# Kernel tuning notes

Measured on AMD Instinct MI355X. Metric: run time of the kernel, lower is better.

The kernel has to match this reference:

```python
import jax, jax.numpy as jnp
import numpy as np
from jax import lax

_R2 = 1.0 / np.sqrt(2.0)
_L = np.array([_R2, _R2]); _Hf = np.array([-_R2, _R2])
F_LL = jnp.asarray(np.outer(_L, _L), jnp.float32)
F_LH = jnp.asarray(np.outer(_L, _Hf), jnp.float32)
F_HL = jnp.asarray(np.outer(_Hf, _L), jnp.float32)
F_HH = jnp.asarray(np.outer(_Hf, _Hf), jnp.float32)
EPS = 1e-5


def _up2(x, f):
    # grouped ConvTranspose2d(k=2, s=2): out[n,c,2i+a,2j+b] = x[n,c,i,j] * f[a,b]
    n, c, h, w = x.shape
    return (x[:, :, :, None, :, None] * f[None, None, None, :, None, :]).reshape(n, c, 2 * h, 2 * w)


def _wave_unpool(ll, lh, hl, hh):
    return _up2(ll, F_LL) + _up2(lh, F_LH) + _up2(hl, F_HL) + _up2(hh, F_HH)


def _rpad(x):
    return jnp.pad(x, ((0, 0), (0, 0), (1, 1), (1, 1)), mode='reflect')


def _conv_relu(x, w, b):
    y = lax.conv_general_dilated(_rpad(x), w, (1, 1), 'VALID',
                                 dimension_numbers=('NCHW', 'OIHW', 'NCHW'))
    return jax.nn.relu(y + b[None, :, None, None])


def _masked_stats(feat, mask):
    # per-(class,n,c) mean/std over NONZERO elements of feat*mask (mask binary)
    nz = (feat != 0).astype(feat.dtype)           # [N,C,H,W]
    cnt = jnp.einsum('khw,nchw->knc', mask, nz)
    s1 = jnp.einsum('khw,nchw->knc', mask, feat)
    s2 = jnp.einsum('khw,nchw->knc', mask, feat * feat)
    m = s1 / jnp.maximum(cnt, 1.0)
    v = (s2 - cnt * m * m) / jnp.maximum(cnt - 1.0, 1.0) + EPS  # unbiased var + eps
    return m, jnp.sqrt(v)


def _global_stats(feat):
    nz = (feat != 0).astype(feat.dtype)
    cnt = nz.sum((2, 3))
    s1 = feat.sum((2, 3))
    s2 = (feat * feat).sum((2, 3))
    m = s1 / jnp.maximum(cnt, 1.0)
    v = (s2 - cnt * m * m) / jnp.maximum(cnt - 1.0, 1.0) + EPS
    return m, jnp.sqrt(v)


def _adain_per_class(content, style, cmask, smask):
    # c_ds=True, s_ds=True branch of AdaIN_per_class, vectorized over classes.
    hc, wc = content.shape[2], content.shape[3]
    hs, ws = style.shape[2], style.shape[3]
    cm = cmask[:, ::2, ::2][:, :hc, :wc]   # MaxPool2d(k=1,s=2) == strided slice
    sm = smask[:, ::2, ::2][:, :hs, :ws]
    cfe = content + EPS
    sfe = style + EPS
    flags = (cmask.max((1, 2)) != 0).astype(content.dtype)   # skip empty content classes
    s_empty = (smask.max((1, 2)) == 0)                       # style-mask-empty -> global style stats
    smm, ssm = _masked_stats(sfe, sm)       # [K,N,C]
    smu, ssu = _global_stats(sfe)           # [N,C]
    s_mean = jnp.where(s_empty[:, None, None], smu[None], smm)
    s_std = jnp.where(s_empty[:, None, None], ssu[None], ssm)
    c_mean, c_std = _masked_stats(cfe, cm)
    # res = sum_k cm_k * ((cfe*cm_k - c_mean)/c_std * s_std + s_mean)
    #     = cfe * sum_k cm_k*scale_k + sum_k cm_k*shift_k   (cm binary)
    scale = flags[:, None, None] * s_std / c_std
    shift = flags[:, None, None] * (s_mean - c_mean * s_std / c_std)
    return cfe * jnp.einsum('khw,knc->nchw', cm, scale) + jnp.einsum('khw,knc->nchw', cm, shift)


def setup_inputs() -> dict:
    key = jax.random.key(0)
    ks = iter(jax.random.split(key, 64))

    def rn(shape, scale=1.0):
        return jax.random.normal(next(ks), shape, jnp.float32) * scale

    inp = {}
    inp['f1'] = rn((4, 128, 128, 128))
    inp['f2'] = rn((4, 512, 32, 32))
    for nm, sh in [('s2', (4, 256, 32, 32)), ('s1', (4, 128, 64, 64)), ('s0', (4, 64, 128, 128))]:
        for band in ('lh', 'hl', 'hh'):
            inp[nm + '_' + band] = rn(sh)
    inp['content_mask'] = jax.random.randint(next(ks), (8, 256, 256), 0, 2).astype(jnp.float32)
    inp['style_mask'] = jax.random.randint(next(ks), (8, 256, 256), 0, 2).astype(jnp.float32)
    for nm, (o, i) in [('w11', (512, 512)), ('w12', (256, 512)), ('w21', (256, 256)),
                       ('w22', (256, 256)), ('w23', (256, 256)), ('w24', (128, 256)),
                       ('w31', (128, 128)), ('w32', (128, 128)), ('w33', (64, 128))]:
        inp[nm] = rn((o, i, 3, 3), 1.0 / np.sqrt(9.0 * i))
        inp['b' + nm[1:]] = jnp.zeros((o,), jnp.float32)
    return inp


def reference(f1, f2, s2_lh, s2_hl, s2_hh, s1_lh, s1_hl, s1_hh, s0_lh, s0_hl, s0_hh,
              content_mask, style_mask,
              w11, b11, w12, b12, w21, b21, w22, b22, w23, b23, w24, b24,
              w31, b31, w32, b32, w33, b33):
    out = _conv_relu(f2, w11, b11)
    out = _conv_relu(out, w12, b12)
    out = _wave_unpool(out, s2_lh, s2_hl, s2_hh)
    out = _rpad(out)[:, :, :s1_hh.shape[2], :s1_hh.shape[3]]
    out = _conv_relu(out, w21, b21)
    out = _conv_relu(out, w22, b22)
    out = _conv_relu(out, w23, b23)
    out = _conv_relu(out, w24, b24)
    out = _wave_unpool(out, s1_lh, s1_hl, s1_hh)
    out = _rpad(out)[:, :, :f1.shape[2], :f1.shape[3]]
    out = _adain_per_class(out, f1, content_mask, style_mask)
    out = _conv_relu(out, w31, b31)
    out = _conv_relu(out, w32, b32)
    out = _conv_relu(out, w33, b33)
    out = _wave_unpool(out, s0_lh, s0_hl, s0_hh)
    return _rpad(out)
```

## Files before the change

### kernel.cpp

```cpp
#include <hip/hip_runtime.h>

#define EPSF 1e-5f

typedef __attribute__((ext_vector_type(4)))  short short4v;
typedef __attribute__((ext_vector_type(8)))  short short8;
typedef __attribute__((ext_vector_type(4)))  float f32x4;
typedef __attribute__((ext_vector_type(16))) float f32x16;

__device__ __forceinline__ unsigned short f2bf(float f) {
  unsigned u = __builtin_bit_cast(unsigned, f);
  unsigned r = (u + 0x7FFFu + ((u >> 16) & 1u)) >> 16;
  return (unsigned short)r;
}
__device__ __forceinline__ float bf2f(unsigned short h) {
  unsigned u = ((unsigned)h) << 16;
  return __builtin_bit_cast(float, u);
}

__global__ void wt_prep(const float* __restrict__ w, unsigned short* __restrict__ wt,
                        int C, int K) {
  int C8 = C >> 3;
  int idx = blockIdx.x * 256 + threadIdx.x;
  if (idx >= K * C8) return;
  int k = idx / C8, ch = idx - k * C8;
  int tap = blockIdx.y;
  const float* src = w + ((size_t)k * C + ch * 8) * 9 + tap;
  short8 v;
#pragma unroll
  for (int cl = 0; cl < 8; ++cl) v[cl] = (short)f2bf(src[cl * 9]);
  *(short8*)(wt + ((size_t)(tap * C8 + ch) * K + k) * 8) = v;
}

__global__ void nchw_to_nc8(const float* __restrict__ in, unsigned short* __restrict__ out,
                            int C8, int HW, int total) {
  int idx = blockIdx.x * 256 + threadIdx.x;
  if (idx >= total) return;
  int pix = idx % HW; int t = idx / HW; int ch = t % C8; int n = t / C8;
  const float* s = in + ((size_t)(n * C8 + ch) * 8) * HW + pix;
  short8 v;
#pragma unroll
  for (int cl = 0; cl < 8; ++cl) v[cl] = (short)f2bf(s[(size_t)cl * HW]);
  *(short8*)(out + (size_t)idx * 8) = v;
}

__global__ __launch_bounds__(256) void conv3x3_mfma(
    const unsigned short* __restrict__ act, const unsigned short* __restrict__ wt,
    const float* __restrict__ bias, unsigned short* __restrict__ out,
    unsigned short* __restrict__ partial, int C, int K, int H, int W, int S) {
  const int C8 = C >> 3, K8 = K >> 3;
  const int HW = H * W;
  const int tid = threadIdx.x;
  const int lane = tid & 63, wid = tid >> 6;
  const int l31 = lane & 31, lhi = lane >> 5;
  const int w0 = blockIdx.x * 16, h0 = blockIdx.y * 16;
  const int kbn = K >> 6;
  int zz = blockIdx.z;
  const int sp = zz % S; zz /= S;
  const int kb = zz % kbn;
  const int n  = zz / kbn;
  const int k0 = kb * 64;

  __shared__ __align__(16) unsigned short smem[24576];
  __shared__ float sbias[64];
  if (tid < 64) sbias[tid] = bias[k0 + tid];

  int g16[6];
#pragma unroll
  for (int it = 0; it < 6; ++it) {
    int slot = it * 256 + wid * 64 + lane;
    int s = slot < 1296 ? slot : 0;
    int chi = s / 324; int r = s - chi * 324;
    int y = r / 18, x = r - y * 18;
    int gy = h0 - 1 + y; gy = gy < 0 ? -gy : (gy >= H ? 2 * H - 2 - gy : gy);
    int gx = w0 - 1 + x; gx = gx < 0 ? -gx : (gx >= W ? 2 * W - 2 - gx : gx);
    g16[it] = ((n * C8 + chi) * H + gy) * W + gx;
  }

  const int pbase = wid * 64;
  int pb[2];
#pragma unroll
  for (int nf = 0; nf < 2; ++nf) {
    int p = pbase + nf * 32 + l31;
    pb[nf] = (p >> 4) * 18 + (p & 15);
  }
  int bb8[2][2];
#pragma unroll
  for (int ks = 0; ks < 2; ++ks)
#pragma unroll
    for (int nf = 0; nf < 2; ++nf)
      bb8[ks][nf] = ((ks * 2 + lhi) * 324 + pb[nf]) * 8;

  const size_t tapStep   = (size_t)C8 * K * 8;
  const size_t chunkStep = (size_t)4 * K * 8;
  const int cps = (C >> 5) / S;
  const int c0 = sp * cps;
  const unsigned short* ap[2][2];
#pragma unroll
  for (int ks = 0; ks < 2; ++ks)
#pragma unroll
    for (int mf = 0; mf < 2; ++mf)
      ap[ks][mf] = wt + ((size_t)(c0 * 4) * K
                  + (size_t)((ks * 2 + lhi) * K + k0 + mf * 32 + l31)) * 8;

  f32x16 acc[2][2] = {};

#define STAGE(BSEL, CI)                                                          \
  {                                                                              \
    _Pragma("unroll")                                                            \
    for (int it = 0; it < 6; ++it) {                                             \
      const unsigned short* g = act + ((size_t)g16[it] + (size_t)(CI) * 4 * HW) * 8; \
      __builtin_amdgcn_global_load_lds(                                          \
          (const __attribute__((address_space(1))) unsigned int*)g,              \
          (__attribute__((address_space(3))) unsigned int*)                      \
              &smem[(BSEL) * 12288 + (it * 256 + wid * 64) * 8],                 \
          16, 0, 0);                                                             \
    }                                                                            \
  }

  STAGE(0, c0)

  for (int i = 0; i < cps; ++i) {
    __syncthreads();
    const int boff = (i & 1) * 12288;
    const unsigned short* aw[2][2];
    short8 acur[2][2], anx[2][2];
#pragma unroll
    for (int ks = 0; ks < 2; ++ks)
#pragma unroll
      for (int mf = 0; mf < 2; ++mf) {
        aw[ks][mf] = ap[ks][mf];
        acur[ks][mf] = *(const short8*)aw[ks][mf];
        aw[ks][mf] += tapStep;
      }
#pragma unroll
    for (int tap = 0; tap < 9; ++tap) {
      if (tap < 8) {
#pragma unroll
        for (int ks = 0; ks < 2; ++ks)
#pragma unroll
          for (int mf = 0; mf < 2; ++mf) {
            anx[ks][mf] = *(const short8*)aw[ks][mf];
            aw[ks][mf] += tapStep;
          }
      }
      if (tap == 7 && i + 1 < cps) STAGE((i & 1) ^ 1, c0 + i + 1)
      const int ty = tap / 3, txx = tap - ty * 3;
      const int toff = (ty * 18 + txx) * 8;
      short8 b[2][2];
#pragma unroll
      for (int ks = 0; ks < 2; ++ks)
#pragma unroll
        for (int nf = 0; nf < 2; ++nf)
          b[nf][ks] = *(const short8*)&smem[boff + bb8[ks][nf] + toff];
#pragma unroll
      for (int ks = 0; ks < 2; ++ks)
#pragma unroll
        for (int mf = 0; mf < 2; ++mf)
#pragma unroll
          for (int nf = 0; nf < 2; ++nf)
            acc[mf][nf] = __builtin_amdgcn_mfma_f32_32x32x16_bf16(
                acur[ks][mf], b[nf][ks], acc[mf][nf], 0, 0, 0);
#pragma unroll
      for (int ks = 0; ks < 2; ++ks)
#pragma unroll
        for (int mf = 0; mf < 2; ++mf)
          acur[ks][mf] = anx[ks][mf];
    }
#pragma unroll
    for (int ks = 0; ks < 2; ++ks)
#pragma unroll
      for (int mf = 0; mf < 2; ++mf)
        ap[ks][mf] += chunkStep;
  }

  if (S > 1) {
    unsigned short* P = partial + (size_t)sp * ((size_t)4 * K * HW);
#pragma unroll
    for (int mf = 0; mf < 2; ++mf)
#pragma unroll
      for (int nf = 0; nf < 2; ++nf) {
        int p = pbase + nf * 32 + l31;
        int gp = (h0 + (p >> 4)) * W + (w0 + (p & 15));
#pragma unroll
        for (int q = 0; q < 4; ++q) {
          size_t ad = ((size_t)(n * K8 + (k0 >> 3) + mf * 4 + q) * HW + gp) * 8 + 4 * lhi;
          short4v v = { (short)f2bf(acc[mf][nf][4 * q]),
                        (short)f2bf(acc[mf][nf][4 * q + 1]),
                        (short)f2bf(acc[mf][nf][4 * q + 2]),
                        (short)f2bf(acc[mf][nf][4 * q + 3]) };
          *(short4v*)(P + ad) = v;
        }
      }
    return;
  }

  __syncthreads();
#pragma unroll
  for (int mf = 0; mf < 2; ++mf)
#pragma unroll
    for (int nf = 0; nf < 2; ++nf) {
      int pix = pbase + nf * 32 + l31;
#pragma unroll
      for (int rp = 0; rp < 8; ++rp) {
        const int r0 = rp * 2;
        int row0 = (r0 & 3) + 8 * (r0 >> 2) + 4 * lhi;
        int c64 = mf * 32 + row0;
        float v0 = acc[mf][nf][r0]     + sbias[c64];
        float v1 = acc[mf][nf][r0 + 1] + sbias[c64 + 1];
        v0 = v0 > 0.f ? v0 : 0.f;
        v1 = v1 > 0.f ? v1 : 0.f;
        unsigned pk = (unsigned)f2bf(v0) | ((unsigned)f2bf(v1) << 16);
        int chh = mf * 4 + (r0 >> 2);
        int clo = (r0 & 3) + 4 * lhi;
        *(unsigned*)&smem[((chh * 256 + pix) * 8 + clo)] = pk;
      }
    }
  __syncthreads();
#pragma unroll
  for (int i = 0; i < 8; ++i) {
    int slot = i * 256 + tid;
    int ch = slot >> 8;
    int p = slot & 255;
    int py = p >> 4, px = p & 15;
    short8 v = *(const short8*)&smem[slot * 8];
    *(short8*)(out + (((size_t)(n * K8 + (k0 >> 3) + ch) * H + h0 + py) * W + w0 + px) * 8) = v;
  }
#undef STAGE
}

__global__ void combine_bias_relu(const unsigned short* __restrict__ P,
                                  const float* __restrict__ bias,
                                  unsigned short* __restrict__ out, int S, int K8, int HW,
                                  int total8) {
  int idx = blockIdx.x * 256 + threadIdx.x;
  if (idx >= total8) return;
  int k8 = (idx / HW) % K8;
  const unsigned short* p = P + (size_t)idx * 8;
  size_t stride = (size_t)total8 * 8;
  float v[8];
#pragma unroll
  for (int c = 0; c < 8; ++c) v[c] = bf2f(p[c]);
  for (int s = 1; s < S; ++s) {
#pragma unroll
    for (int c = 0; c < 8; ++c) v[c] += bf2f(p[(size_t)s * stride + c]);
  }
  short8 r;
#pragma unroll
  for (int c = 0; c < 8; ++c) {
    float x = v[c] + bias[k8 * 8 + c];
    x = x > 0.f ? x : 0.f;
    r[c] = (short)f2bf(x);
  }
  *(short8*)(out + (size_t)idx * 8) = r;
}

__global__ void unpool_shift_fused(const unsigned short* __restrict__ P,
                                   const float* __restrict__ bias,
                                   const float* __restrict__ lh, const float* __restrict__ hl,
                                   const float* __restrict__ hh, unsigned short* __restrict__ out,
                                   int C8, int Hh, int Wh, int S, int total) {
  int idx = blockIdx.x * 256 + threadIdx.x;
  if (idx >= total) return;
  const int Ho = 2 * Hh, Wo = 2 * Wh;
  int j = idx % Wo; int t = idx / Wo;
  int i = t % Ho; t /= Ho;
  int ch = t % C8; int n = t / C8;
  int si = (i == 0) ? 1 : i - 1;
  int sj = (j == 0) ? 1 : j - 1;
  float sa = (si & 1) ? 1.f : -1.f;
  float sb = (sj & 1) ? 1.f : -1.f;
  int hy = si >> 1, hx = sj >> 1;
  size_t HWh = (size_t)Hh * Wh;
  const size_t sstr = (size_t)4 * (C8 * 8) * HWh;
  size_t lbase = ((size_t)(n * C8 + ch) * HWh + hy * Wh + hx) * 8;
  float ll[8];
  {
    short8 v0 = *(const short8*)(P + lbase);
#pragma unroll
    for (int cl = 0; cl < 8; ++cl) ll[cl] = bf2f((unsigned short)v0[cl]);
  }
  for (int s = 1; s < S; ++s) {
    short8 vs = *(const short8*)(P + (size_t)s * sstr + lbase);
#pragma unroll
    for (int cl = 0; cl < 8; ++cl) ll[cl] += bf2f((unsigned short)vs[cl]);
  }
#pragma unroll
  for (int cl = 0; cl < 8; ++cl) {
    float x = ll[cl] + bias[ch * 8 + cl];
    ll[cl] = x > 0.f ? x : 0.f;
  }
  size_t bb = ((size_t)(n * C8 + ch) * 8 * Hh + hy) * Wh + hx;
  short8 res;
#pragma unroll
  for (int cl = 0; cl < 8; ++cl) {
    float v = 0.5f * (ll[cl] + sb * lh[bb + cl * HWh] + sa * hl[bb + cl * HWh]
                      + sa * sb * hh[bb + cl * HWh]);
    res[cl] = (short)f2bf(v);
  }
  *(short8*)(out + (size_t)idx * 8) = res;
}

__global__ void unpool_rpad_final_v3(const unsigned short* __restrict__ ll,
                                     const float* __restrict__ lh, const float* __restrict__ hl,
                                     const float* __restrict__ hh, float* __restrict__ out) {
  const int img = blockIdx.y;
  int idx = blockIdx.x * 256 + threadIdx.x;
  if (idx >= 130 * 129) return;
  int g = idx / 129, jm = idx - g * 129;
  const int n = img >> 6, c = img & 63;

  int hy = (g == 0) ? 0 : (g == 129 ? 127 : g - 1);
  int hx0 = (jm == 0) ? 0 : jm - 1;
  int hx1 = (jm == 128) ? 127 : jm;

  size_t lb = ((size_t)(n * 8 + (c >> 3)) * 16384 + hy * 128) * 8 + (c & 7);
  float ll0 = bf2f(ll[lb + hx0 * 8]);
  float ll1 = bf2f(ll[lb + hx1 * 8]);

  size_t bb = ((size_t)img * 128 + hy) * 128;
  float l0 = lh[bb + hx0], G0 = hl[bb + hx0], h0 = hh[bb + hx0];
  float l1 = lh[bb + hx1], G1 = hl[bb + hx1], h1 = hh[bb + hx1];

  float e0 = ll0 + l0, f0 = G0 + h0;
  float e1 = ll1 - l1, f1 = G1 - h1;
  float2 rm = make_float2(0.5f * (e0 - f0), 0.5f * (e1 - f1));
  float2 rp = make_float2(0.5f * (e0 + f0), 0.5f * (e1 + f1));

  float* obase = out + (size_t)img * 258 * 258 + 2 * jm;
  if (g == 0) {
    *(float2*)&obase[0] = rp;
  } else if (g == 129) {
    *(float2*)&obase[(size_t)257 * 258] = rm;
  } else {
    *(float2*)&obase[(size_t)(2 * g - 1) * 258] = rm;
    *(float2*)&obase[(size_t)(2 * g) * 258]     = rp;
  }
}

__global__ void pack_masks(const float* __restrict__ cmask, const float* __restrict__ smask,
                           unsigned* __restrict__ cbits, unsigned* __restrict__ sbits) {
  int idx = blockIdx.x * 256 + threadIdx.x;
  if (idx >= 16384) return;
  int h = idx >> 7, w = idx & 127;
  unsigned cb = 0, sb = 0;
#pragma unroll
  for (int k = 0; k < 8; ++k) {
    int off = (k * 256 + 2 * h) * 256 + 2 * w;
    if (cmask[off] != 0.f) cb |= (1u << k);
    if (smask[off] != 0.f) sb |= (1u << k);
  }
  cbits[idx] = cb;
  sbits[idx] = sb;
}

__global__ __launch_bounds__(1024) void mask_flags(
    const float* __restrict__ cmask, const float* __restrict__ smask,
    float* __restrict__ flagc, float* __restrict__ sany) {
  int k = blockIdx.x;
  const float* cm = cmask + (size_t)k * 65536;
  const float* sm = smask + (size_t)k * 65536;
  int ca = 0, sa = 0;
  for (int i = threadIdx.x; i < 65536; i += 1024) {
    ca |= (cm[i] != 0.f);
    sa |= (sm[i] != 0.f);
  }
#pragma unroll
  for (int off = 32; off > 0; off >>= 1) {
    ca |= __shfl_xor(ca, off, 64);
    sa |= __shfl_xor(sa, off, 64);
  }
  __shared__ int rc[16], rs[16];
  int wv = threadIdx.x >> 6;
  if ((threadIdx.x & 63) == 0) { rc[wv] = ca; rs[wv] = sa; }
  __syncthreads();
  if (threadIdx.x == 0) {
    int c = 0, s = 0;
#pragma unroll
    for (int i = 0; i < 16; ++i) { c |= rc[i]; s |= rs[i]; }
    flagc[k] = c ? 1.f : 0.f;
    sany[k]  = s ? 1.f : 0.f;
  }
}

__global__ __launch_bounds__(256) void masked_stats_bf16(
    const unsigned short* __restrict__ feat, const unsigned* __restrict__ bits,
    float* __restrict__ outp, int NC) {
  constexpr int NV = 24;
  int b = blockIdx.x; int n = b >> 7, c = b & 127;
  const int sp = blockIdx.y;
  const unsigned short* f = feat + (size_t)(n * 16 + (c >> 3)) * 16384 * 8 + (c & 7);
  float acc[NV];
#pragma unroll
  for (int j = 0; j < NV; ++j) acc[j] = 0.f;
  const int p0 = sp * 4096;
  for (int it = 0; it < 16; ++it) {
    int i = p0 + it * 256 + threadIdx.x;
    float v = bf2f(f[(size_t)i * 8]) + EPSF;
    float nz = (v != 0.f) ? 1.f : 0.f;
    float v2 = v * v;
    unsigned m = bits[i];
#pragma unroll
    for (int k = 0; k < 8; ++k) {
      float mk = (float)((m >> k) & 1u);
      acc[k * 3 + 0] += mk * nz;
      acc[k * 3 + 1] += mk * v;
      acc[k * 3 + 2] += mk * v2;
    }
  }
#pragma unroll
  for (int j = 0; j < NV; ++j) {
    float v = acc[j];
#pragma unroll
    for (int off = 32; off > 0; off >>= 1) v += __shfl_xor(v, off, 64);
    acc[j] = v;
  }
  __shared__ float red[4][NV];
  int lane = threadIdx.x & 63, wv = threadIdx.x >> 6;
  if (lane == 0) {
#pragma unroll
    for (int j = 0; j < NV; ++j) red[wv][j] = acc[j];
  }
  __syncthreads();
  int tid = threadIdx.x;
  if (tid < NV) {
    float s = red[0][tid] + red[1][tid] + red[2][tid] + red[3][tid];
    outp[(sp * NV + tid) * NC + b] = s;
  }
}

__global__ __launch_bounds__(256) void masked_stats_f32g(
    const float* __restrict__ feat, const unsigned* __restrict__ bits,
    float* __restrict__ sstp, float* __restrict__ gstp, int NC) {
  constexpr int NV = 27;
  const int b = blockIdx.x;
  const int sp = blockIdx.y;
  const float* f = feat + (size_t)b * 16384;
  float acc[NV];
#pragma unroll
  for (int j = 0; j < NV; ++j) acc[j] = 0.f;
  const int p0 = sp * 4096;
#pragma unroll 1
  for (int it = 0; it < 4; ++it) {
    int p = p0 + it * 1024 + threadIdx.x * 4;
    float4 v4 = *(const float4*)&f[p];
    uint4 m4 = *(const uint4*)&bits[p];
#pragma unroll
    for (int e = 0; e < 4; ++e) {
      float v = (&v4.x)[e] + EPSF;
      unsigned m = (&m4.x)[e];
      float nz = (v != 0.f) ? 1.f : 0.f;
      float v2 = v * v;
#pragma unroll
      for (int k = 0; k < 8; ++k) {
        float mk = (float)((m >> k) & 1u);
        acc[k * 3 + 0] += mk * nz;
        acc[k * 3 + 1] += mk * v;
        acc[k * 3 + 2] += mk * v2;
      }
      acc[24] += nz; acc[25] += v; acc[26] += v2;
    }
  }
#pragma unroll
  for (int j = 0; j < NV; ++j) {
    float v = acc[j];
#pragma unroll
    for (int off = 32; off > 0; off >>= 1) v += __shfl_xor(v, off, 64);
    acc[j] = v;
  }
  __shared__ float red[4][NV];
  int lane = threadIdx.x & 63, wv = threadIdx.x >> 6;
  if (lane == 0) {
#pragma unroll
    for (int j = 0; j < NV; ++j) red[wv][j] = acc[j];
  }
  __syncthreads();
  int tid = threadIdx.x;
  if (tid < NV) {
    float s = red[0][tid] + red[1][tid] + red[2][tid] + red[3][tid];
    if (tid < 24) sstp[(sp * 24 + tid) * NC + b] = s;
    else gstp[(sp * 3 + (tid - 24)) * NC + b] = s;
  }
}

__global__ void finalize_ss(const float* __restrict__ cstp, const float* __restrict__ sstp,
                            const float* __restrict__ gstp, const float* __restrict__ flagc,
                            const float* __restrict__ sany,
                            float* __restrict__ scal, float* __restrict__ shft, int NC) {
  int idx = blockIdx.x * blockDim.x + threadIdx.x;
  if (idx >= 8 * NC) return;
  int k = idx / NC, b = idx - k * NC;
  bool useg = (sany[k] == 0.f);
  float ccnt = 0.f, cs1 = 0.f, cs2 = 0.f, scnt = 0.f, ss1 = 0.f, ss2 = 0.f;
#pragma unroll
  for (int s = 0; s < 4; ++s) {
    const float* cp = cstp + s * 24 * NC;
    ccnt += cp[(k * 3 + 0) * NC + b];
    cs1  += cp[(k * 3 + 1) * NC + b];
    cs2  += cp[(k * 3 + 2) * NC + b];
    if (useg) {
      const float* gp = gstp + s * 3 * NC;
      scnt += gp[0 * NC + b]; ss1 += gp[1 * NC + b]; ss2 += gp[2 * NC + b];
    } else {
      const float* spp = sstp + s * 24 * NC;
      scnt += spp[(k * 3 + 0) * NC + b];
      ss1  += spp[(k * 3 + 1) * NC + b];
      ss2  += spp[(k * 3 + 2) * NC + b];
    }
  }
  float cmn  = cs1 / fmaxf(ccnt, 1.f);
  float cvv  = (cs2 - ccnt * cmn * cmn) / fmaxf(ccnt - 1.f, 1.f) + EPSF;
  float cstd = sqrtf(cvv);
  float smn  = ss1 / fmaxf(scnt, 1.f);
  float svv  = (ss2 - scnt * smn * smn) / fmaxf(scnt - 1.f, 1.f) + EPSF;
  float sstd = sqrtf(svv);
  float fl = flagc[k];
  float r  = sstd / cstd;
  scal[idx] = fl * r;
  shft[idx] = fl * (smn - cmn * r);
}

__global__ void adain_apply_nc8(const unsigned short* __restrict__ content,
                                const unsigned* __restrict__ bits,
                                const float* __restrict__ scal, const float* __restrict__ shft,
                                unsigned short* __restrict__ out) {
  int ch = blockIdx.x & 15, n = blockIdx.x >> 4;
  __shared__ float ssc[8][8], ssh[8][8];
  if (threadIdx.x < 64) {
    int k = threadIdx.x >> 3, cl = threadIdx.x & 7;
    int c = ch * 8 + cl;
    ssc[k][cl] = scal[k * 512 + n * 128 + c];
    ssh[k][cl] = shft[k * 512 + n * 128 + c];
  }
  __syncthreads();
  const unsigned short* src = content + (size_t)blockIdx.x * 16384 * 8;
  unsigned short* dst = out + (size_t)blockIdx.x * 16384 * 8;
  const int p0 = blockIdx.y * 1024;
  for (int p = p0 + threadIdx.x; p < p0 + 1024; p += 256) {
    unsigned m = bits[p];
    float sc[8], sh[8];
#pragma unroll
    for (int cl = 0; cl < 8; ++cl) { sc[cl] = 0.f; sh[cl] = 0.f; }
    for (int k = 0; k < 8; ++k) {
      if ((m >> k) & 1u) {
#pragma unroll
        for (int cl = 0; cl < 8; ++cl) { sc[cl] += ssc[k][cl]; sh[cl] += ssh[k][cl]; }
      }
    }
    short8 v = *(const short8*)(src + (size_t)p * 8);
    short8 r;
#pragma unroll
    for (int cl = 0; cl < 8; ++cl) {
      float f = bf2f((unsigned short)v[cl]) + EPSF;
      r[cl] = (short)f2bf(f * sc[cl] + sh[cl]);
    }
    *(short8*)(dst + (size_t)p * 8) = r;
  }
}

static void launch_conv(const unsigned short* act, const unsigned short* wt,
                        const float* bias, unsigned short* out, unsigned short* partial,
                        int C, int K, int H, int W, int S, bool combine, hipStream_t st) {
  dim3 g(W / 16, H / 16, 4 * (K / 64) * S);
  conv3x3_mfma<<<g, 256, 0, st>>>(act, wt, bias, out, partial, C, K, H, W, S);
  if (S > 1 && combine) {
    int total8 = 4 * (K >> 3) * H * W;
    combine_bias_relu<<<(total8 + 255) / 256, 256, 0, st>>>(
        partial, bias, out, S, K >> 3, H * W, total8);
  }
}

extern "C" void kernel_launch(void* const* d_in, const int* in_sizes, int n_in,
                              void* d_out, int out_size, void* d_ws, size_t ws_size,
                              hipStream_t stream) {
  const float* f1   = (const float*)d_in[0];
  const float* f2   = (const float*)d_in[1];
  const float* s2lh = (const float*)d_in[2];
  const float* s2hl = (const float*)d_in[3];
  const float* s2hh = (const float*)d_in[4];
  const float* s1lh = (const float*)d_in[5];
  const float* s1hl = (const float*)d_in[6];
  const float* s1hh = (const float*)d_in[7];
  const float* s0lh = (const float*)d_in[8];
  const float* s0hl = (const float*)d_in[9];
  const float* s0hh = (const float*)d_in[10];
  const float* cmask = (const float*)d_in[11];
  const float* smask = (const float*)d_in[12];
  const float* w11 = (const float*)d_in[13]; const float* b11 = (const float*)d_in[14];
  const float* w12 = (const float*)d_in[15]; const float* b12 = (const float*)d_in[16];
  const float* w21 = (const float*)d_in[17]; const float* b21 = (const float*)d_in[18];
  const float* w22 = (const float*)d_in[19]; const float* b22 = (const float*)d_in[20];
  const float* w23 = (const float*)d_in[21]; const float* b23 = (const float*)d_in[22];
  const float* w24 = (const float*)d_in[23]; const float* b24 = (const float*)d_in[24];
  const float* w31 = (const float*)d_in[25]; const float* b31 = (const float*)d_in[26];
  const float* w32 = (const float*)d_in[27]; const float* b32 = (const float*)d_in[28];
  const float* w33 = (const float*)d_in[29]; const float* b33 = (const float*)d_in[30];

  unsigned short* A = (unsigned short*)d_out;
  unsigned short* B = A + 8388608;
  unsigned short* P = (unsigned short*)((char*)d_out + 33554432);

  char* wsb = (char*)d_ws;
  unsigned short* wtb = (unsigned short*)wsb;
  const size_t o11 = 0,        o12 = 2359296, o21 = 3538944, o22 = 4128768,
               o23 = 4718592,  o24 = 5308416, o31 = 5603328, o32 = 5750784,
               o33 = 5898240;
  unsigned short* f2c = (unsigned short*)(wsb + 11943936);
  unsigned* cbits = (unsigned*)(wsb + 16138240);
  unsigned* sbits = (unsigned*)(wsb + 16203776);
  float* cstp = (float*)(wsb + 16269312);
  float* sstp = (float*)(wsb + 16465920);
  float* gstp = (float*)(wsb + 16662528);
  float* scal = (float*)(wsb + 16687104);
  float* shft = (float*)(wsb + 16703488);
  float* flagc = (float*)(wsb + 16719872);
  float* sany  = (float*)(wsb + 16719904);
  unsigned short* t12 = (unsigned short*)wsb;

  const int NC = 512;

  wt_prep<<<dim3((512 * 64 + 255) / 256, 9), 256, 0, stream>>>(w11, wtb + o11, 512, 512);
  wt_prep<<<dim3((256 * 64 + 255) / 256, 9), 256, 0, stream>>>(w12, wtb + o12, 512, 256);
  wt_prep<<<dim3((256 * 32 + 255) / 256, 9), 256, 0, stream>>>(w21, wtb + o21, 256, 256);
  wt_prep<<<dim3((256 * 32 + 255) / 256, 9), 256, 0, stream>>>(w22, wtb + o22, 256, 256);
  wt_prep<<<dim3((256 * 32 + 255) / 256, 9), 256, 0, stream>>>(w23, wtb + o23, 256, 256);
  wt_prep<<<dim3((128 * 32 + 255) / 256, 9), 256, 0, stream>>>(w24, wtb + o24, 256, 128);
  wt_prep<<<dim3((128 * 16 + 255) / 256, 9), 256, 0, stream>>>(w31, wtb + o31, 128, 128);
  wt_prep<<<dim3((128 * 16 + 255) / 256, 9), 256, 0, stream>>>(w32, wtb + o32, 128, 128);
  wt_prep<<<dim3(( 64 * 16 + 255) / 256, 9), 256, 0, stream>>>(w33, wtb + o33, 128,  64);

  nchw_to_nc8<<<(262144 + 255) / 256, 256, 0, stream>>>(f2, f2c, 64, 1024, 262144);

  pack_masks<<<64, 256, 0, stream>>>(cmask, smask, cbits, sbits);
  mask_flags<<<8, 1024, 0, stream>>>(cmask, smask, flagc, sany);

  launch_conv(f2c, wtb + o11, b11, A, P, 512, 512, 32, 32, 4, true, stream);
  launch_conv(A,   wtb + o12, b12, B, P, 512, 256, 32, 32, 8, false, stream);
  unpool_shift_fused<<<(524288 + 255) / 256, 256, 0, stream>>>(
      P, b12, s2lh, s2hl, s2hh, A, 32, 32, 32, 8, 524288);
  launch_conv(A,   wtb + o21, b21, B, P, 256, 256, 64, 64, 2, true, stream);
  launch_conv(B,   wtb + o22, b22, A, P, 256, 256, 64, 64, 2, true, stream);
  launch_conv(A,   wtb + o23, b23, B, P, 256, 256, 64, 64, 2, true, stream);
  launch_conv(B,   wtb + o24, b24, A, P, 256, 128, 64, 64, 4, false, stream);
  unpool_shift_fused<<<(1048576 + 255) / 256, 256, 0, stream>>>(
      P, b24, s1lh, s1hl, s1hh, B, 16, 64, 64, 4, 1048576);

  masked_stats_bf16<<<dim3(512, 4), 256, 0, stream>>>(B, cbits, cstp, NC);
  masked_stats_f32g<<<dim3(512, 4), 256, 0, stream>>>(f1, sbits, sstp, gstp, NC);
  finalize_ss<<<16, 256, 0, stream>>>(cstp, sstp, gstp, flagc, sany, scal, shft, NC);
  adain_apply_nc8<<<dim3(64, 16), 256, 0, stream>>>(B, cbits, scal, shft, A);

  launch_conv(A, wtb + o31, b31, B, P, 128, 128, 128, 128, 1, true, stream);
  launch_conv(B, wtb + o32, b32, A, P, 128, 128, 128, 128, 1, true, stream);
  launch_conv(A, wtb + o33, b33, t12, P, 128, 64, 128, 128, 2, true, stream);

  unpool_rpad_final_v3<<<dim3(66, 256), 256, 0, stream>>>(
      t12, s0lh, s0hl, s0hh, (float*)d_out);
}
```

Before: 446.1 us.

## Add 128-output-channel conv tile variant for 64x64 layers with deeper split-K

Adds a conv kernel in which each block computes 128 output channels over a 16x16 pixel tile, using 4x2 MFMA fragments per wave. Each staged activation tile is therefore reused across twice as many output channels. The four 64x64 convs switch to this kernel with split-K doubled so the grid stays the same size. The trade-off is more partial-sum traffic in the combine and unpool steps, plus higher register pressure from the larger accumulator set.

```diff
diff --git a/kernel.cpp b/kernel.cpp
--- a/kernel.cpp
+++ b/kernel.cpp
@@ -225,6 +225,146 @@
     short8 v = *(const short8*)&smem[slot * 8];
     *(short8*)(out + (((size_t)(n * K8 + (k0 >> 3) + ch) * H + h0 + py) * W + w0 + px) * 8) = v;
   }
+#undef STAGE
+}
+
+__global__ __launch_bounds__(256) void conv3x3_mfma_w128(
+    const unsigned short* __restrict__ act, const unsigned short* __restrict__ wt,
+    const float* __restrict__ bias, unsigned short* __restrict__ out,
+    unsigned short* __restrict__ partial, int C, int K, int H, int W, int S) {
+  const int C8 = C >> 3, K8 = K >> 3;
+  const int HW = H * W;
+  const int tid = threadIdx.x;
+  const int lane = tid & 63, wid = tid >> 6;
+  const int l31 = lane & 31, lhi = lane >> 5;
+  const int w0 = blockIdx.x * 16, h0 = blockIdx.y * 16;
+  const int kbn = K >> 7;
+  int zz = blockIdx.z;
+  const int sp = zz % S; zz /= S;
+  const int kb = zz % kbn;
+  const int n  = zz / kbn;
+  const int k0 = kb * 128;
+
+  __shared__ __align__(16) unsigned short smem[24576];
+
+  int g16[6];
+#pragma unroll
+  for (int it = 0; it < 6; ++it) {
+    int slot = it * 256 + wid * 64 + lane;
+    int s = slot < 1296 ? slot : 0;
+    int chi = s / 324; int r = s - chi * 324;
+    int y = r / 18, x = r - y * 18;
+    int gy = h0 - 1 + y; gy = gy < 0 ? -gy : (gy >= H ? 2 * H - 2 - gy : gy);
+    int gx = w0 - 1 + x; gx = gx < 0 ? -gx : (gx >= W ? 2 * W - 2 - gx : gx);
+    g16[it] = ((n * C8 + chi) * H + gy) * W + gx;
+  }
+
+  const int pbase = wid * 64;
+  int pb[2];
+#pragma unroll
+  for (int nf = 0; nf < 2; ++nf) {
+    int p = pbase + nf * 32 + l31;
+    pb[nf] = (p >> 4) * 18 + (p & 15);
+  }
+  int bb8[2][2];
+#pragma unroll
+  for (int ks = 0; ks < 2; ++ks)
+#pragma unroll
+    for (int nf = 0; nf < 2; ++nf)
+      bb8[ks][nf] = ((ks * 2 + lhi) * 324 + pb[nf]) * 8;
+
+  const size_t tapStep   = (size_t)C8 * K * 8;
+  const size_t chunkStep = (size_t)4 * K * 8;
+  const int cps = (C >> 5) / S;
+  const int c0 = sp * cps;
+  int aoff[2][4];
+#pragma unroll
+  for (int ks = 0; ks < 2; ++ks)
+#pragma unroll
+    for (int mf = 0; mf < 4; ++mf)
+      aoff[ks][mf] = ((ks * 2 + lhi) * K + k0 + mf * 32 + l31) * 8;
+  const unsigned short* abase = wt + (size_t)(c0 * 4) * K * 8;
+
+  f32x16 acc[4][2] = {};
+
+#define STAGE(BSEL, CI)                                                          \
+  {                                                                              \
+    _Pragma("unroll")                                                            \
+    for (int it = 0; it < 6; ++it) {                                             \
+      const unsigned short* g = act + ((size_t)g16[it] + (size_t)(CI) * 4 * HW) * 8; \
+      __builtin_amdgcn_global_load_lds(                                          \
+          (const __attribute__((address_space(1))) unsigned int*)g,              \
+          (__attribute__((address_space(3))) unsigned int*)                      \
+              &smem[(BSEL) * 12288 + (it * 256 + wid * 64) * 8],                 \
+          16, 0, 0);                                                             \
+    }                                                                            \
+  }
+
+  STAGE(0, c0)
+
+  for (int i = 0; i < cps; ++i) {
+    __syncthreads();
+    const int boff = (i & 1) * 12288;
+    const unsigned short* atap = abase + tapStep;
+    short8 acur[2][4], anx[2][4];
+#pragma unroll
+    for (int ks = 0; ks < 2; ++ks)
+#pragma unroll
+      for (int mf = 0; mf < 4; ++mf)
+        acur[ks][mf] = *(const short8*)(abase + aoff[ks][mf]);
+#pragma unroll
+    for (int tap = 0; tap < 9; ++tap) {
+      if (tap < 8) {
+#pragma unroll
+        for (int ks = 0; ks < 2; ++ks)
+#pragma unroll
+          for (int mf = 0; mf < 4; ++mf)
+            anx[ks][mf] = *(const short8*)(atap + aoff[ks][mf]);
+        atap += tapStep;
+      }
+      if (tap == 7 && i + 1 < cps) STAGE((i & 1) ^ 1, c0 + i + 1)
+      const int ty = tap / 3, txx = tap - ty * 3;
+      const int toff = (ty * 18 + txx) * 8;
+      short8 b[2][2];
+#pragma unroll
+      for (int ks = 0; ks < 2; ++ks)
+#pragma unroll
+        for (int nf = 0; nf < 2; ++nf)
+          b[nf][ks] = *(const short8*)&smem[boff + bb8[ks][nf] + toff];
+#pragma unroll
+      for (int ks = 0; ks < 2; ++ks)
+#pragma unroll
+        for (int mf = 0; mf < 4; ++mf)
+#pragma unroll
+          for (int nf = 0; nf < 2; ++nf)
+            acc[mf][nf] = __builtin_amdgcn_mfma_f32_32x32x16_bf16(
+                acur[ks][mf], b[nf][ks], acc[mf][nf], 0, 0, 0);
+#pragma unroll
+      for (int ks = 0; ks < 2; ++ks)
+#pragma unroll
+        for (int mf = 0; mf < 4; ++mf)
+          acur[ks][mf] = anx[ks][mf];
+    }
+    abase += chunkStep;
+  }
+
+  unsigned short* P = partial + (size_t)sp * ((size_t)4 * K * HW);
+#pragma unroll
+  for (int mf = 0; mf < 4; ++mf)
+#pragma unroll
+    for (int nf = 0; nf < 2; ++nf) {
+      int p = pbase + nf * 32 + l31;
+      int gp = (h0 + (p >> 4)) * W + (w0 + (p & 15));
+#pragma unroll
+      for (int q = 0; q < 4; ++q) {
+        size_t ad = ((size_t)(n * K8 + (k0 >> 3) + mf * 4 + q) * HW + gp) * 8 + 4 * lhi;
+        short4v v = { (short)f2bf(acc[mf][nf][4 * q]),
+                      (short)f2bf(acc[mf][nf][4 * q + 1]),
+                      (short)f2bf(acc[mf][nf][4 * q + 2]),
+                      (short)f2bf(acc[mf][nf][4 * q + 3]) };
+        *(short4v*)(P + ad) = v;
+      }
+    }
 #undef STAGE
 }
 
@@ -563,6 +703,18 @@
   dim3 g(W / 16, H / 16, 4 * (K / 64) * S);
   conv3x3_mfma<<<g, 256, 0, st>>>(act, wt, bias, out, partial, C, K, H, W, S);
   if (S > 1 && combine) {
+    int total8 = 4 * (K >> 3) * H * W;
+    combine_bias_relu<<<(total8 + 255) / 256, 256, 0, st>>>(
+        partial, bias, out, S, K >> 3, H * W, total8);
+  }
+}
+
+static void launch_conv_w128(const unsigned short* act, const unsigned short* wt,
+                             const float* bias, unsigned short* out, unsigned short* partial,
+                             int C, int K, int H, int W, int S, bool combine, hipStream_t st) {
+  dim3 g(W / 16, H / 16, 4 * (K / 128) * S);
+  conv3x3_mfma_w128<<<g, 256, 0, st>>>(act, wt, bias, out, partial, C, K, H, W, S);
+  if (combine) {
     int total8 = 4 * (K >> 3) * H * W;
     combine_bias_relu<<<(total8 + 255) / 256, 256, 0, st>>>(
         partial, bias, out, S, K >> 3, H * W, total8);
@@ -637,12 +789,12 @@
   launch_conv(A,   wtb + o12, b12, B, P, 512, 256, 32, 32, 8, false, stream);
   unpool_shift_fused<<<(524288 + 255) / 256, 256, 0, stream>>>(
       P, b12, s2lh, s2hl, s2hh, A, 32, 32, 32, 8, 524288);
-  launch_conv(A,   wtb + o21, b21, B, P, 256, 256, 64, 64, 2, true, stream);
-  launch_conv(B,   wtb + o22, b22, A, P, 256, 256, 64, 64, 2, true, stream);
-  launch_conv(A,   wtb + o23, b23, B, P, 256, 256, 64, 64, 2, true, stream);
-  launch_conv(B,   wtb + o24, b24, A, P, 256, 128, 64, 64, 4, false, stream);
+  launch_conv_w128(A, wtb + o21, b21, B, P, 256, 256, 64, 64, 4, true, stream);
+  launch_conv_w128(B, wtb + o22, b22, A, P, 256, 256, 64, 64, 4, true, stream);
+  launch_conv_w128(A, wtb + o23, b23, B, P, 256, 256, 64, 64, 4, true, stream);
+  launch_conv_w128(B, wtb + o24, b24, A, P, 256, 128, 64, 64, 8, false, stream);
   unpool_shift_fused<<<(1048576 + 255) / 256, 256, 0, stream>>>(
-      P, b24, s1lh, s1hl, s1hh, B, 16, 64, 64, 4, 1048576);
+      P, b24, s1lh, s1hl, s1hh, B, 16, 64, 64, 8, 1048576);
 
   masked_stats_bf16<<<dim3(512, 4), 256, 0, stream>>>(B, cbits, cstp, NC);
   masked_stats_f32g<<<dim3(512, 4), 256, 0, stream>>>(f1, sbits, sstp, gstp, NC);
```

New measurement: 518.2 us. 16.2% more time.
